# Kernel optimization log

Measured on AMD Instinct MI355X. Metric: run time of the kernel, lower is better.

The kernel has to match this reference:

```python
import jax, jax.numpy as jnp
import numpy as np

N_NODES = 50000
N_EDGES = 800000
NFEAT, NHID, NOUT = 128, 128, 64


def _glorot(key, shape):
    lim = 1.0 / np.sqrt(shape[0])
    return jax.random.uniform(key, shape, jnp.float32, -lim, lim)


def setup_inputs() -> dict:
    key = jax.random.key(0)
    ks = jax.random.split(key, 12)
    x = jax.random.normal(ks[0], (N_NODES, NFEAT), jnp.float32)
    edge_src = jax.random.randint(ks[1], (N_EDGES,), 0, N_NODES, jnp.int32)
    edge_dst = jax.random.randint(ks[2], (N_EDGES,), 0, N_NODES, jnp.int32)
    edge_w = jax.random.uniform(ks[3], (N_EDGES,), jnp.float32)  # normalized adj values
    # layer params: nfeat->nhid, nhid->nhid, nhid->nhid, nhid->nout
    W0, b0 = _glorot(ks[4], (NFEAT, NHID)), jnp.zeros((NHID,), jnp.float32)
    W1, b1 = _glorot(ks[5], (NHID, NHID)), jnp.zeros((NHID,), jnp.float32)
    W2, b2 = _glorot(ks[6], (NHID, NHID)), jnp.zeros((NHID,), jnp.float32)
    W3, b3 = _glorot(ks[7], (NHID, NOUT)), jnp.zeros((NOUT,), jnp.float32)
    return dict(x=x, edge_src=edge_src, edge_dst=edge_dst, edge_w=edge_w,
                W0=W0, b0=b0, W1=W1, b1=b1, W2=W2, b2=b2, W3=W3, b3=b3)


def _gcn_layer(h, src, dst, w, W, b):
    # support = h @ W ; out = A @ support + b  (A given as weighted edge list)
    support = h @ W                               # [N, d_out]
    msgs = support[src] * w[:, None]              # [E, d_out] gather + scale
    agg = jax.ops.segment_sum(msgs, dst, num_segments=N_NODES)  # scatter-add
    return agg + b


def reference(x, edge_src, edge_dst, edge_w, W0, b0, W1, b1, W2, b2, W3, b3):
    # eval mode: dropout is identity
    h = jax.nn.relu(_gcn_layer(x, edge_src, edge_dst, edge_w, W0, b0))
    h = jax.nn.relu(_gcn_layer(h, edge_src, edge_dst, edge_w, W1, b1))
    h = jax.nn.relu(_gcn_layer(h, edge_src, edge_dst, edge_w, W2, b2))
    h = _gcn_layer(h, edge_src, edge_dst, edge_w, W3, b3)  # no relu on last layer
    return h
```

## Files before the change

### kernel.cpp

```cpp
#include <hip/hip_runtime.h>


constexpr int NN = 50000;
constexpr int NE = 800000;
constexpr int NB = (NN + 127) >> 7;
constexpr int CAP = 4608;
constexpr int PART_CHUNK = 4096;
constexpr int PART_GRID = (NE + PART_CHUNK - 1) / PART_CHUNK;

typedef __attribute__((ext_vector_type(8))) short bf16x8;
typedef __attribute__((ext_vector_type(4))) float floatx4;
typedef __attribute__((ext_vector_type(2))) float floatx2;

__device__ inline unsigned short f2bf(float f) {
    unsigned u = __float_as_uint(f);
    u += 0x7fffu + ((u >> 16) & 1u);
    return (unsigned short)(u >> 16);
}
__device__ inline float bflo(unsigned v) { return __uint_as_float(v << 16); }
__device__ inline float bfhi(unsigned v) { return __uint_as_float(v & 0xffff0000u); }
__device__ inline unsigned char f2fp8(float f) {
    return (unsigned char)(__builtin_amdgcn_cvt_pk_fp8_f32(f, f, 0, false) & 0xff);
}


__global__ __launch_bounds__(256) void k_part(
        const int* __restrict__ src, const int* __restrict__ dst,
        const float* __restrict__ w, int* __restrict__ bfill,
        int2* __restrict__ ep) {
    __shared__ int hist[NB], base[NB], off[NB];
    int tid = threadIdx.x;
    for (int b = tid; b < NB; b += 256) { hist[b] = 0; off[b] = 0; }
    __syncthreads();

    int e0 = blockIdx.x * PART_CHUNK;
    int  sreg[16]; int wreg[16]; short breg[16];
#pragma unroll
    for (int i = 0; i < 16; ++i) {
        int e = e0 + i * 256 + tid;
        if (e < NE) {
            int d = dst[e];
            int b = d >> 7;
            sreg[i] = (src[e] & 0xffff) | ((d & 127) << 16);
            wreg[i] = __float_as_int(w[e]);
            breg[i] = (short)b;
            atomicAdd(&hist[b], 1);
        } else breg[i] = -1;
    }
    __syncthreads();
    for (int b = tid; b < NB; b += 256)
        base[b] = b * CAP + atomicAdd(&bfill[b], hist[b]);
    __syncthreads();
#pragma unroll
    for (int i = 0; i < 16; ++i) {
        if (breg[i] >= 0) {
            int b = breg[i];
            int p = atomicAdd(&off[b], 1);
            ep[base[b] + p] = make_int2(sreg[i], wreg[i]);
        }
    }
}

__global__ __launch_bounds__(256) void k_sort(
        const int2* __restrict__ ep, const int* __restrict__ bfill,
        unsigned* __restrict__ es, int2* __restrict__ begend) {
    __shared__ int cnt[128], base[128], fl[128];
    __shared__ int s_total;
    int b  = blockIdx.x;
    int n0 = b << 7;
    int nn = min(128, NN - n0);
    int t  = threadIdx.x;
    if (t < 128) { cnt[t] = 0; fl[t] = 0; }
    __syncthreads();
    int bbase = b * CAP;
    int beg = bbase, end = bbase + bfill[b];
    for (int e = beg + t; e < end; e += 256)
        atomicAdd(&cnt[(ep[e].x >> 16) & 127], 1);
    __syncthreads();
    int cp = (t < 128) ? ((cnt[t] + 15) & ~15) : 0;
    if (t < 128) base[t] = cp;
    __syncthreads();
    for (int off = 1; off < 128; off <<= 1) {
        int add = (t >= off && t < 128) ? base[t - off] : 0;
        __syncthreads();
        if (t < 128) base[t] += add;
        __syncthreads();
    }
    if (t == 127) s_total = base[127];
    __syncthreads();
    int total = s_total;
    for (int i = t; i < total + 16; i += 256) es[bbase + i] = 0u;
    if (t < nn) {
        int off = base[t] - cp;
        begend[n0 + t] = make_int2(bbase + off, bbase + off + cp);
    }
    __syncthreads();
    for (int e = beg + t; e < end; e += 256) {
        int2 v = ep[e];
        int d = (v.x >> 16) & 127;
        int off = base[d] - ((cnt[d] + 15) & ~15);
        int pos = bbase + off + atomicAdd(&fl[d], 1);
        es[pos] = (unsigned)(v.x & 0xffff) |
                  ((unsigned)f2bf(__int_as_float(v.y)) << 16);
    }
}


__global__ void k_prep(
        const float* __restrict__ W0, const float* __restrict__ W1,
        const float* __restrict__ W2, const float* __restrict__ W3,
        unsigned short* __restrict__ T0, unsigned short* __restrict__ T1,
        unsigned short* __restrict__ T2, unsigned short* __restrict__ T3,
        int* __restrict__ bfill) {
    int b = blockIdx.x;
    if (b == 448) {
        for (int i = threadIdx.x; i < NB; i += 128) bfill[i] = 0;
        return;
    }
    const float* W; unsigned short* T; int N, n;
    if (b < 128)      { W = W0; T = T0; N = 128; n = b; }
    else if (b < 256) { W = W1; T = T1; N = 128; n = b - 128; }
    else if (b < 384) { W = W2; T = T2; N = 128; n = b - 256; }
    else              { W = W3; T = T3; N = 64;  n = b - 384; }
    int k = threadIdx.x;
    T[n * 128 + k] = f2bf(W[(size_t)k * N + n]);
}


__device__ inline bf16x8 ldA_f32(const float* A, size_t off) {
    float4 u = *(const float4*)&A[off];
    float4 v = *(const float4*)&A[off + 4];
    bf16x8 r;
    r[0] = (short)f2bf(u.x); r[1] = (short)f2bf(u.y);
    r[2] = (short)f2bf(u.z); r[3] = (short)f2bf(u.w);
    r[4] = (short)f2bf(v.x); r[5] = (short)f2bf(v.y);
    r[6] = (short)f2bf(v.z); r[7] = (short)f2bf(v.w);
    return r;
}

__global__ __launch_bounds__(256) void k_gemm0(
        const float* __restrict__ A,
        const unsigned short* __restrict__ Wt,
        unsigned char* __restrict__ C,
        int M) {
    constexpr int STR = 136;
    __shared__ unsigned short sWt[128 * STR];

    const int tid = threadIdx.x;
#pragma unroll
    for (int i = 0; i < 8; ++i) {
        int c = i * 256 + tid;
        int row = c >> 4, col = (c & 15) * 8;
        *(uint4*)&sWt[row * STR + col] = *(const uint4*)&Wt[row * 128 + col];
    }

    const int wv = tid >> 6;
    const int ln = tid & 63;
    const int m  = ln & 15;
    const int qd = ln >> 4;

    int gr  = blockIdx.x * 64 + wv * 16 + m;
    int grc = (gr < M) ? gr : (M - 1);
    bf16x8 af[4];
#pragma unroll
    for (int s = 0; s < 4; ++s)
        af[s] = ldA_f32(A, (size_t)grc * 128 + s * 32 + qd * 8);

    __syncthreads();

    floatx4 acc[8];
#pragma unroll
    for (int c = 0; c < 8; ++c) {
        acc[c] = (floatx4){0.f, 0.f, 0.f, 0.f};
#pragma unroll
        for (int s = 0; s < 4; ++s) {
            bf16x8 bf = *(const bf16x8*)&sWt[(c * 16 + m) * STR + s * 32 + qd * 8];
            acc[c] = __builtin_amdgcn_mfma_f32_16x16x32_bf16(af[s], bf, acc[c], 0, 0, 0);
        }
    }

    int row0 = blockIdx.x * 64 + wv * 16 + qd * 4;
#pragma unroll
    for (int c = 0; c < 8; ++c)
#pragma unroll
        for (int r = 0; r < 4; ++r) {
            int row = row0 + r;
            if (row < M) C[(size_t)row * 128 + c * 16 + m] = f2fp8(acc[c][r]);
        }
}


#define FMAP8(W, R)                                                             \
    { floatx2 p0 = __builtin_amdgcn_cvt_pk_f32_fp8((int)(R).x, false);          \
      floatx2 p1 = __builtin_amdgcn_cvt_pk_f32_fp8((int)(R).x, true);           \
      floatx2 p2 = __builtin_amdgcn_cvt_pk_f32_fp8((int)(R).y, false);          \
      floatx2 p3 = __builtin_amdgcn_cvt_pk_f32_fp8((int)(R).y, true);           \
      acc[0] = fmaf(W, p0.x, acc[0]); acc[1] = fmaf(W, p0.y, acc[1]);           \
      acc[2] = fmaf(W, p1.x, acc[2]); acc[3] = fmaf(W, p1.y, acc[3]);           \
      acc[4] = fmaf(W, p2.x, acc[4]); acc[5] = fmaf(W, p2.y, acc[5]);           \
      acc[6] = fmaf(W, p3.x, acc[6]); acc[7] = fmaf(W, p3.y, acc[7]); }

template<int NOUT, typename CT>
__global__ __launch_bounds__(128, 4) void k_fused(
        const unsigned char* __restrict__ sup,
        const int2* __restrict__ begend, const unsigned* __restrict__ es,
        const float* __restrict__ bias,
        const unsigned short* __restrict__ Wt,
        CT* __restrict__ C,
        int M) {
    constexpr int NT  = NOUT / 16;
    constexpr int STR = 136;
    __shared__ unsigned short hT[16 * STR];

    const int tid = threadIdx.x;
    const int wv  = tid >> 6;
    const int ln  = tid & 63;
    const int g   = ln >> 4;
    const int l   = ln & 15;

    const int n0 = blockIdx.x * 16;
    int2 be = begend[n0 + wv * 8];

    for (int nn = 0; nn < 8; ++nn) {
        int n = n0 + wv * 8 + nn;
        int beg = be.x, endp = be.y;
        if (nn < 7) be = begend[n + 1];
        float acc[8] = {0.f, 0.f, 0.f, 0.f, 0.f, 0.f, 0.f, 0.f};
        if (endp > beg) {
            int e = beg;
            uint4 mv = *(const uint4*)&es[e + 4 * g];
            for (;;) {
                uint2 r0 = *(const uint2*)&sup[(size_t)(mv.x & 0xffffu) * 128 + l * 8];
                uint2 r1 = *(const uint2*)&sup[(size_t)(mv.y & 0xffffu) * 128 + l * 8];
                uint2 r2 = *(const uint2*)&sup[(size_t)(mv.z & 0xffffu) * 128 + l * 8];
                uint2 r3 = *(const uint2*)&sup[(size_t)(mv.w & 0xffffu) * 128 + l * 8];
                float w0 = bfhi(mv.x), w1 = bfhi(mv.y);
                float w2 = bfhi(mv.z), w3 = bfhi(mv.w);
                e += 16;
                bool more = e < endp;
                uint4 mn = *(const uint4*)&es[e + 4 * g];
                FMAP8(w0, r0); FMAP8(w1, r1); FMAP8(w2, r2); FMAP8(w3, r3);
                mv = mn;
                if (!more) break;
            }
#pragma unroll
            for (int f = 0; f < 8; ++f) {
                acc[f] += __shfl_xor(acc[f], 16, 64);
                acc[f] += __shfl_xor(acc[f], 32, 64);
            }
        }
        if (g == 0) {
            unsigned pk[4];
#pragma unroll
            for (int q = 0; q < 4; ++q) {
                float a0 = fmaxf(acc[2 * q]     + bias[l * 8 + 2 * q],     0.f);
                float a1 = fmaxf(acc[2 * q + 1] + bias[l * 8 + 2 * q + 1], 0.f);
                pk[q] = (unsigned)f2bf(a0) | ((unsigned)f2bf(a1) << 16);
            }
            *(uint4*)&hT[(wv * 8 + nn) * STR + l * 8] = *(uint4*)pk;
        }
    }
    __syncthreads();

    const int m_ = ln & 15, qd = ln >> 4;
    const int c0 = wv * (NT / 2);
    bf16x8 af[4];
#pragma unroll
    for (int s = 0; s < 4; ++s)
        af[s] = *(const bf16x8*)&hT[m_ * STR + s * 32 + qd * 8];

    floatx4 acc2[NT / 2];
#pragma unroll
    for (int c = 0; c < NT / 2; ++c) {
        acc2[c] = (floatx4){0.f, 0.f, 0.f, 0.f};
#pragma unroll
        for (int s = 0; s < 4; ++s) {
            bf16x8 bf = *(const bf16x8*)&Wt[(size_t)((c0 + c) * 16 + m_) * 128 + s * 32 + qd * 8];
            acc2[c] = __builtin_amdgcn_mfma_f32_16x16x32_bf16(af[s], bf, acc2[c], 0, 0, 0);
        }
    }
    int row0 = n0 + qd * 4;
#pragma unroll
    for (int c = 0; c < NT / 2; ++c)
#pragma unroll
        for (int r = 0; r < 4; ++r) {
            int row = row0 + r;
            if (row < M) {
                if constexpr (sizeof(CT) == 1)
                    C[(size_t)row * NOUT + (c0 + c) * 16 + m_] = (CT)f2fp8(acc2[c][r]);
                else
                    C[(size_t)row * NOUT + (c0 + c) * 16 + m_] = (CT)f2bf(acc2[c][r]);
            }
        }
}


#define FMA8(W, R)                                                              \
    acc[0] = fmaf(W, bflo((R).x), acc[0]); acc[1] = fmaf(W, bfhi((R).x), acc[1]); \
    acc[2] = fmaf(W, bflo((R).y), acc[2]); acc[3] = fmaf(W, bfhi((R).y), acc[3]); \
    acc[4] = fmaf(W, bflo((R).z), acc[4]); acc[5] = fmaf(W, bfhi((R).z), acc[5]); \
    acc[6] = fmaf(W, bflo((R).w), acc[6]); acc[7] = fmaf(W, bfhi((R).w), acc[7]);

__global__ __launch_bounds__(256, 4) void k_agg64(
        const unsigned short* __restrict__ sup,
        const int2* __restrict__ begend, const unsigned* __restrict__ es,
        const float* __restrict__ bias, float* __restrict__ out) {
    int n  = blockIdx.x * 4 + (threadIdx.x >> 6);
    int ln = threadIdx.x & 63;
    int g  = ln >> 3, l = ln & 7;
    int2 be = begend[n];
    int beg = be.x, endp = be.y;
    float acc[8] = {0.f, 0.f, 0.f, 0.f, 0.f, 0.f, 0.f, 0.f};
    if (endp > beg) {
        int e = beg;
        uint2 mv = *(const uint2*)&es[e + 2 * g];
        for (;;) {
            uint4 r0 = *(const uint4*)&sup[(size_t)(mv.x & 0xffffu) * 64 + l * 8];
            uint4 r1 = *(const uint4*)&sup[(size_t)(mv.y & 0xffffu) * 64 + l * 8];
            float w0 = bfhi(mv.x), w1 = bfhi(mv.y);
            e += 16;
            bool more = e < endp;
            uint2 mn = *(const uint2*)&es[e + 2 * g];
            FMA8(w0, r0); FMA8(w1, r1);
            mv = mn;
            if (!more) break;
        }
    }
#pragma unroll
    for (int f = 0; f < 8; ++f) {
        acc[f] += __shfl_xor(acc[f], 8, 64);
        acc[f] += __shfl_xor(acc[f], 16, 64);
        acc[f] += __shfl_xor(acc[f], 32, 64);
    }
    if (g == 0) {
        float4 o0 = make_float4(acc[0] + bias[l * 8],     acc[1] + bias[l * 8 + 1],
                                acc[2] + bias[l * 8 + 2], acc[3] + bias[l * 8 + 3]);
        float4 o1 = make_float4(acc[4] + bias[l * 8 + 4], acc[5] + bias[l * 8 + 5],
                                acc[6] + bias[l * 8 + 6], acc[7] + bias[l * 8 + 7]);
        *(float4*)&out[(size_t)n * 64 + l * 8]     = o0;
        *(float4*)&out[(size_t)n * 64 + l * 8 + 4] = o1;
    }
}


extern "C" void kernel_launch(void* const* d_in, const int* in_sizes, int n_in,
                              void* d_out, int out_size, void* d_ws, size_t ws_size,
                              hipStream_t stream) {
    (void)in_sizes; (void)n_in; (void)out_size; (void)ws_size;

    const float* x    = (const float*)d_in[0];
    const int*   esrc = (const int*)d_in[1];
    const int*   edst = (const int*)d_in[2];
    const float* ew   = (const float*)d_in[3];
    const float* W0   = (const float*)d_in[4];
    const float* b0   = (const float*)d_in[5];
    const float* W1   = (const float*)d_in[6];
    const float* b1   = (const float*)d_in[7];
    const float* W2   = (const float*)d_in[8];
    const float* b2   = (const float*)d_in[9];
    const float* W3   = (const float*)d_in[10];
    const float* b3   = (const float*)d_in[11];

    char* p = (char*)d_ws;
    auto alloc = [&](size_t bytes) {
        char* r = p;
        p += (bytes + 511) & ~size_t(511);
        return r;
    };
    int*      bfill  = (int*)     alloc((size_t)NB * 4);
    int2*     begend = (int2*)    alloc((size_t)NN * 8);
    int2*     ep     = (int2*)    alloc((size_t)NB * CAP * 8);
    unsigned* es     = (unsigned*)alloc((size_t)NB * CAP * 4);
    unsigned char*  s8a = (unsigned char*) alloc((size_t)NN * 128);
    unsigned char*  s8b = (unsigned char*) alloc((size_t)NN * 128);
    unsigned short* s16 = (unsigned short*)alloc((size_t)NN * 64 * 2);
    unsigned short* Wt0 = (unsigned short*)alloc((size_t)128 * 128 * 2);
    unsigned short* Wt1 = (unsigned short*)alloc((size_t)128 * 128 * 2);
    unsigned short* Wt2 = (unsigned short*)alloc((size_t)128 * 128 * 2);
    unsigned short* Wt3 = (unsigned short*)alloc((size_t)64 * 128 * 2);

    k_prep<<<449, 128, 0, stream>>>(W0, W1, W2, W3, Wt0, Wt1, Wt2, Wt3, bfill);
    k_part<<<PART_GRID, 256, 0, stream>>>(esrc, edst, ew, bfill, ep);
    k_sort<<<NB, 256, 0, stream>>>(ep, bfill, es, begend);

    const int g0_grid = (NN + 63) / 64;
    const int f_grid  = (NN + 15) / 16;
    const int a_grid  = (NN + 3) / 4;

    k_gemm0<<<g0_grid, 256, 0, stream>>>(x, Wt0, s8a, NN);
    k_fused<128, unsigned char><<<f_grid, 128, 0, stream>>>(s8a, begend, es, b0, Wt1, s8b, NN);
    k_fused<128, unsigned char><<<f_grid, 128, 0, stream>>>(s8b, begend, es, b1, Wt2, s8a, NN);
    k_fused<64, unsigned short><<<f_grid, 128, 0, stream>>>(s8a, begend, es, b2, Wt3, s16, NN);
    k_agg64<<<a_grid, 256, 0, stream>>>(s16, begend, es, b3, (float*)d_out);
}
```

Baseline: 239.4 us.

## Unfuse aggregation and GEMM, split support features into column slices

Replaces the fused aggregate-then-GEMM kernel with separate aggregation and MFMA GEMM kernels, and stores the support matrices as two column slices. Each aggregation block handles one slice, so every gathered row is narrower and the working set of the random gather is halved per pass, which should help cache hit rates. Nontemporal loads and stores are used for edge metadata and the intermediate hidden buffer. The cost is an extra bf16 hidden buffer written and re-read between kernels, plus more kernel launches.

```diff
diff --git a/kernel.cpp b/kernel.cpp
--- a/kernel.cpp
+++ b/kernel.cpp
@@ -11,6 +11,7 @@
 typedef __attribute__((ext_vector_type(8))) short bf16x8;
 typedef __attribute__((ext_vector_type(4))) float floatx4;
 typedef __attribute__((ext_vector_type(2))) float floatx2;
+typedef __attribute__((ext_vector_type(4))) unsigned int uintx4;
 
 __device__ inline unsigned short f2bf(float f) {
     unsigned u = __float_as_uint(f);
@@ -185,7 +186,77 @@
 #pragma unroll
         for (int r = 0; r < 4; ++r) {
             int row = row0 + r;
-            if (row < M) C[(size_t)row * 128 + c * 16 + m] = f2fp8(acc[c][r]);
+            if (row < M) {
+                int col = c * 16 + m;
+                int sl  = col >> 6;
+                C[(size_t)sl * NN * 64 + (size_t)row * 64 + (col & 63)] =
+                    f2fp8(acc[c][r]);
+            }
+        }
+}
+
+
+template<int NO, typename CT>
+__global__ __launch_bounds__(256) void k_gemmh(
+        const unsigned short* __restrict__ A,
+        const unsigned short* __restrict__ Wt,
+        CT* __restrict__ C,
+        int M) {
+    constexpr int STR = 136;
+    __shared__ unsigned short sWt[NO * STR];
+
+    const int tid = threadIdx.x;
+#pragma unroll
+    for (int i = 0; i < NO / 16; ++i) {
+        int c = i * 256 + tid;
+        int row = c >> 4, col = (c & 15) * 8;
+        *(uint4*)&sWt[row * STR + col] = *(const uint4*)&Wt[row * 128 + col];
+    }
+
+    const int wv = tid >> 6;
+    const int ln = tid & 63;
+    const int m  = ln & 15;
+    const int qd = ln >> 4;
+
+    int gr  = blockIdx.x * 64 + wv * 16 + m;
+    int grc = (gr < M) ? gr : (M - 1);
+    bf16x8 af[4];
+#pragma unroll
+    for (int s = 0; s < 4; ++s)
+        af[s] = __builtin_nontemporal_load(
+            (const bf16x8*)&A[(size_t)grc * 128 + s * 32 + qd * 8]);
+
+    __syncthreads();
+
+    floatx4 acc[NO / 16];
+#pragma unroll
+    for (int c = 0; c < NO / 16; ++c) {
+        acc[c] = (floatx4){0.f, 0.f, 0.f, 0.f};
+#pragma unroll
+        for (int s = 0; s < 4; ++s) {
+            bf16x8 bf = *(const bf16x8*)&sWt[(c * 16 + m) * STR + s * 32 + qd * 8];
+            acc[c] = __builtin_amdgcn_mfma_f32_16x16x32_bf16(af[s], bf, acc[c], 0, 0, 0);
+        }
+    }
+
+    int row0 = blockIdx.x * 64 + wv * 16 + qd * 4;
+#pragma unroll
+    for (int c = 0; c < NO / 16; ++c)
+#pragma unroll
+        for (int r = 0; r < 4; ++r) {
+            int row = row0 + r;
+            if (row < M) {
+                int col = c * 16 + m;
+                if constexpr (sizeof(CT) == 1) {
+                    int sl = col >> 6;
+                    C[(size_t)sl * NN * 64 + (size_t)row * 64 + (col & 63)] =
+                        (CT)f2fp8(acc[c][r]);
+                } else {
+                    int sl = col >> 5;
+                    C[(size_t)sl * NN * 32 + (size_t)row * 32 + (col & 31)] =
+                        (CT)f2bf(acc[c][r]);
+                }
+            }
         }
 }
 
@@ -200,145 +271,131 @@
       acc[4] = fmaf(W, p2.x, acc[4]); acc[5] = fmaf(W, p2.y, acc[5]);           \
       acc[6] = fmaf(W, p3.x, acc[6]); acc[7] = fmaf(W, p3.y, acc[7]); }
 
-template<int NOUT, typename CT>
-__global__ __launch_bounds__(128, 4) void k_fused(
+__global__ __launch_bounds__(128, 8) void k_aggh(
         const unsigned char* __restrict__ sup,
         const int2* __restrict__ begend, const unsigned* __restrict__ es,
         const float* __restrict__ bias,
-        const unsigned short* __restrict__ Wt,
-        CT* __restrict__ C,
-        int M) {
-    constexpr int NT  = NOUT / 16;
-    constexpr int STR = 136;
-    __shared__ unsigned short hT[16 * STR];
-
-    const int tid = threadIdx.x;
-    const int wv  = tid >> 6;
-    const int ln  = tid & 63;
-    const int g   = ln >> 4;
-    const int l   = ln & 15;
-
-    const int n0 = blockIdx.x * 16;
-    int2 be = begend[n0 + wv * 8];
+        unsigned short* __restrict__ h) {
+    const int bid  = blockIdx.x;
+    const int sl   = bid & 1;
+    const int tile = bid >> 1;
+    const int tid  = threadIdx.x;
+    const int wv = tid >> 6, ln = tid & 63;
+    const int g = ln >> 3, l = ln & 7;
+    const unsigned char* supS = sup + (size_t)sl * NN * 64;
+    const float* biasS = bias + sl * 64;
+
+    const int n0 = tile * 16 + wv * 8;
+    unsigned long long beq = __builtin_nontemporal_load(
+        (const unsigned long long*)&begend[n0]);
 
     for (int nn = 0; nn < 8; ++nn) {
-        int n = n0 + wv * 8 + nn;
-        int beg = be.x, endp = be.y;
-        if (nn < 7) be = begend[n + 1];
+        const int n = n0 + nn;
+        int beg  = (int)(unsigned)beq;
+        int endp = (int)(unsigned)(beq >> 32);
+        if (nn < 7)
+            beq = __builtin_nontemporal_load(
+                (const unsigned long long*)&begend[n + 1]);
         float acc[8] = {0.f, 0.f, 0.f, 0.f, 0.f, 0.f, 0.f, 0.f};
         if (endp > beg) {
             int e = beg;
-            uint4 mv = *(const uint4*)&es[e + 4 * g];
+            unsigned long long mv = __builtin_nontemporal_load(
+                (const unsigned long long*)&es[e + 2 * g]);
             for (;;) {
-                uint2 r0 = *(const uint2*)&sup[(size_t)(mv.x & 0xffffu) * 128 + l * 8];
-                uint2 r1 = *(const uint2*)&sup[(size_t)(mv.y & 0xffffu) * 128 + l * 8];
-                uint2 r2 = *(const uint2*)&sup[(size_t)(mv.z & 0xffffu) * 128 + l * 8];
-                uint2 r3 = *(const uint2*)&sup[(size_t)(mv.w & 0xffffu) * 128 + l * 8];
-                float w0 = bfhi(mv.x), w1 = bfhi(mv.y);
-                float w2 = bfhi(mv.z), w3 = bfhi(mv.w);
+                unsigned lo = (unsigned)mv, hi = (unsigned)(mv >> 32);
+                uint2 r0 = *(const uint2*)&supS[(size_t)(lo & 0xffffu) * 64 + l * 8];
+                uint2 r1 = *(const uint2*)&supS[(size_t)(hi & 0xffffu) * 64 + l * 8];
+                float w0 = bfhi(lo), w1 = bfhi(hi);
                 e += 16;
                 bool more = e < endp;
-                uint4 mn = *(const uint4*)&es[e + 4 * g];
-                FMAP8(w0, r0); FMAP8(w1, r1); FMAP8(w2, r2); FMAP8(w3, r3);
+                unsigned long long mn = __builtin_nontemporal_load(
+                    (const unsigned long long*)&es[e + 2 * g]);
+                FMAP8(w0, r0); FMAP8(w1, r1);
                 mv = mn;
                 if (!more) break;
             }
 #pragma unroll
             for (int f = 0; f < 8; ++f) {
+                acc[f] += __shfl_xor(acc[f], 8, 64);
                 acc[f] += __shfl_xor(acc[f], 16, 64);
                 acc[f] += __shfl_xor(acc[f], 32, 64);
             }
         }
         if (g == 0) {
-            unsigned pk[4];
+            uintx4 pk;
 #pragma unroll
             for (int q = 0; q < 4; ++q) {
-                float a0 = fmaxf(acc[2 * q]     + bias[l * 8 + 2 * q],     0.f);
-                float a1 = fmaxf(acc[2 * q + 1] + bias[l * 8 + 2 * q + 1], 0.f);
+                float a0 = fmaxf(acc[2 * q]     + biasS[l * 8 + 2 * q],     0.f);
+                float a1 = fmaxf(acc[2 * q + 1] + biasS[l * 8 + 2 * q + 1], 0.f);
                 pk[q] = (unsigned)f2bf(a0) | ((unsigned)f2bf(a1) << 16);
             }
-            *(uint4*)&hT[(wv * 8 + nn) * STR + l * 8] = *(uint4*)pk;
-        }
-    }
-    __syncthreads();
-
-    const int m_ = ln & 15, qd = ln >> 4;
-    const int c0 = wv * (NT / 2);
-    bf16x8 af[4];
-#pragma unroll
-    for (int s = 0; s < 4; ++s)
-        af[s] = *(const bf16x8*)&hT[m_ * STR + s * 32 + qd * 8];
-
-    floatx4 acc2[NT / 2];
-#pragma unroll
-    for (int c = 0; c < NT / 2; ++c) {
-        acc2[c] = (floatx4){0.f, 0.f, 0.f, 0.f};
-#pragma unroll
-        for (int s = 0; s < 4; ++s) {
-            bf16x8 bf = *(const bf16x8*)&Wt[(size_t)((c0 + c) * 16 + m_) * 128 + s * 32 + qd * 8];
-            acc2[c] = __builtin_amdgcn_mfma_f32_16x16x32_bf16(af[s], bf, acc2[c], 0, 0, 0);
-        }
-    }
-    int row0 = n0 + qd * 4;
-#pragma unroll
-    for (int c = 0; c < NT / 2; ++c)
-#pragma unroll
-        for (int r = 0; r < 4; ++r) {
-            int row = row0 + r;
-            if (row < M) {
-                if constexpr (sizeof(CT) == 1)
-                    C[(size_t)row * NOUT + (c0 + c) * 16 + m_] = (CT)f2fp8(acc2[c][r]);
-                else
-                    C[(size_t)row * NOUT + (c0 + c) * 16 + m_] = (CT)f2bf(acc2[c][r]);
-            }
-        }
-}
-
-
-#define FMA8(W, R)                                                              \
+            __builtin_nontemporal_store(
+                pk, (uintx4*)&h[(size_t)n * 128 + sl * 64 + l * 8]);
+        }
+    }
+}
+
+
+#define FMA4(W, R)                                                              \
     acc[0] = fmaf(W, bflo((R).x), acc[0]); acc[1] = fmaf(W, bfhi((R).x), acc[1]); \
-    acc[2] = fmaf(W, bflo((R).y), acc[2]); acc[3] = fmaf(W, bfhi((R).y), acc[3]); \
-    acc[4] = fmaf(W, bflo((R).z), acc[4]); acc[5] = fmaf(W, bfhi((R).z), acc[5]); \
-    acc[6] = fmaf(W, bflo((R).w), acc[6]); acc[7] = fmaf(W, bfhi((R).w), acc[7]);
-
-__global__ __launch_bounds__(256, 4) void k_agg64(
+    acc[2] = fmaf(W, bflo((R).y), acc[2]); acc[3] = fmaf(W, bfhi((R).y), acc[3]);
+
+__global__ __launch_bounds__(128, 8) void k_aggo(
         const unsigned short* __restrict__ sup,
         const int2* __restrict__ begend, const unsigned* __restrict__ es,
         const float* __restrict__ bias, float* __restrict__ out) {
-    int n  = blockIdx.x * 4 + (threadIdx.x >> 6);
-    int ln = threadIdx.x & 63;
-    int g  = ln >> 3, l = ln & 7;
-    int2 be = begend[n];
-    int beg = be.x, endp = be.y;
-    float acc[8] = {0.f, 0.f, 0.f, 0.f, 0.f, 0.f, 0.f, 0.f};
-    if (endp > beg) {
-        int e = beg;
-        uint2 mv = *(const uint2*)&es[e + 2 * g];
-        for (;;) {
-            uint4 r0 = *(const uint4*)&sup[(size_t)(mv.x & 0xffffu) * 64 + l * 8];
-            uint4 r1 = *(const uint4*)&sup[(size_t)(mv.y & 0xffffu) * 64 + l * 8];
-            float w0 = bfhi(mv.x), w1 = bfhi(mv.y);
-            e += 16;
-            bool more = e < endp;
-            uint2 mn = *(const uint2*)&es[e + 2 * g];
-            FMA8(w0, r0); FMA8(w1, r1);
-            mv = mn;
-            if (!more) break;
-        }
-    }
-#pragma unroll
-    for (int f = 0; f < 8; ++f) {
-        acc[f] += __shfl_xor(acc[f], 8, 64);
-        acc[f] += __shfl_xor(acc[f], 16, 64);
-        acc[f] += __shfl_xor(acc[f], 32, 64);
-    }
-    if (g == 0) {
-        float4 o0 = make_float4(acc[0] + bias[l * 8],     acc[1] + bias[l * 8 + 1],
-                                acc[2] + bias[l * 8 + 2], acc[3] + bias[l * 8 + 3]);
-        float4 o1 = make_float4(acc[4] + bias[l * 8 + 4], acc[5] + bias[l * 8 + 5],
-                                acc[6] + bias[l * 8 + 6], acc[7] + bias[l * 8 + 7]);
-        *(float4*)&out[(size_t)n * 64 + l * 8]     = o0;
-        *(float4*)&out[(size_t)n * 64 + l * 8 + 4] = o1;
+    const int bid  = blockIdx.x;
+    const int sl   = bid & 1;
+    const int tile = bid >> 1;
+    const int tid  = threadIdx.x;
+    const int wv = tid >> 6, ln = tid & 63;
+    const int g = ln >> 3, l = ln & 7;
+    const unsigned short* supS = sup + (size_t)sl * NN * 32;
+    const float* biasS = bias + sl * 32;
+
+    const int n0 = tile * 16 + wv * 8;
+    unsigned long long beq = __builtin_nontemporal_load(
+        (const unsigned long long*)&begend[n0]);
+
+    for (int nn = 0; nn < 8; ++nn) {
+        const int n = n0 + nn;
+        int beg  = (int)(unsigned)beq;
+        int endp = (int)(unsigned)(beq >> 32);
+        if (nn < 7)
+            beq = __builtin_nontemporal_load(
+                (const unsigned long long*)&begend[n + 1]);
+        float acc[4] = {0.f, 0.f, 0.f, 0.f};
+        if (endp > beg) {
+            int e = beg;
+            unsigned long long mv = __builtin_nontemporal_load(
+                (const unsigned long long*)&es[e + 2 * g]);
+            for (;;) {
+                unsigned lo = (unsigned)mv, hi = (unsigned)(mv >> 32);
+                uint2 r0 = *(const uint2*)&supS[(size_t)(lo & 0xffffu) * 32 + l * 4];
+                uint2 r1 = *(const uint2*)&supS[(size_t)(hi & 0xffffu) * 32 + l * 4];
+                float w0 = bfhi(lo), w1 = bfhi(hi);
+                e += 16;
+                bool more = e < endp;
+                unsigned long long mn = __builtin_nontemporal_load(
+                    (const unsigned long long*)&es[e + 2 * g]);
+                FMA4(w0, r0); FMA4(w1, r1);
+                mv = mn;
+                if (!more) break;
+            }
+#pragma unroll
+            for (int f = 0; f < 4; ++f) {
+                acc[f] += __shfl_xor(acc[f], 8, 64);
+                acc[f] += __shfl_xor(acc[f], 16, 64);
+                acc[f] += __shfl_xor(acc[f], 32, 64);
+            }
+        }
+        if (g == 0) {
+            float4 o = make_float4(acc[0] + biasS[l * 4],
+                                   acc[1] + biasS[l * 4 + 1],
+                                   acc[2] + biasS[l * 4 + 2],
+                                   acc[3] + biasS[l * 4 + 3]);
+            *(float4*)&out[(size_t)n * 64 + sl * 32 + l * 4] = o;
+        }
     }
 }
 
@@ -371,9 +428,10 @@
     int2*     begend = (int2*)    alloc((size_t)NN * 8);
     int2*     ep     = (int2*)    alloc((size_t)NB * CAP * 8);
     unsigned* es     = (unsigned*)alloc((size_t)NB * CAP * 4);
-    unsigned char*  s8a = (unsigned char*) alloc((size_t)NN * 128);
-    unsigned char*  s8b = (unsigned char*) alloc((size_t)NN * 128);
-    unsigned short* s16 = (unsigned short*)alloc((size_t)NN * 64 * 2);
+    unsigned char*  s8a  = (unsigned char*) alloc((size_t)NN * 128);
+    unsigned char*  s8b  = (unsigned char*) alloc((size_t)NN * 128);
+    unsigned short* s16  = (unsigned short*)alloc((size_t)NN * 64 * 2);
+    unsigned short* hbuf = (unsigned short*)alloc((size_t)NN * 128 * 2);
     unsigned short* Wt0 = (unsigned short*)alloc((size_t)128 * 128 * 2);
     unsigned short* Wt1 = (unsigned short*)alloc((size_t)128 * 128 * 2);
     unsigned short* Wt2 = (unsigned short*)alloc((size_t)128 * 128 * 2);
@@ -383,13 +441,15 @@
     k_part<<<PART_GRID, 256, 0, stream>>>(esrc, edst, ew, bfill, ep);
     k_sort<<<NB, 256, 0, stream>>>(ep, bfill, es, begend);
 
-    const int g0_grid = (NN + 63) / 64;
-    const int f_grid  = (NN + 15) / 16;
-    const int a_grid  = (NN + 3) / 4;
-
-    k_gemm0<<<g0_grid, 256, 0, stream>>>(x, Wt0, s8a, NN);
-    k_fused<128, unsigned char><<<f_grid, 128, 0, stream>>>(s8a, begend, es, b0, Wt1, s8b, NN);
-    k_fused<128, unsigned char><<<f_grid, 128, 0, stream>>>(s8b, begend, es, b1, Wt2, s8a, NN);
-    k_fused<64, unsigned short><<<f_grid, 128, 0, stream>>>(s8a, begend, es, b2, Wt3, s16, NN);
-    k_agg64<<<a_grid, 256, 0, stream>>>(s16, begend, es, b3, (float*)d_out);
-}
+    const int g_gemm = (NN + 63) / 64;
+    const int g_agg  = (NN / 16) * 2;
+
+    k_gemm0<<<g_gemm, 256, 0, stream>>>(x, Wt0, s8a, NN);
+    k_aggh<<<g_agg, 128, 0, stream>>>(s8a, begend, es, b0, hbuf);
+    k_gemmh<128, unsigned char><<<g_gemm, 256, 0, stream>>>(hbuf, Wt1, s8b, NN);
+    k_aggh<<<g_agg, 128, 0, stream>>>(s8b, begend, es, b1, hbuf);
+    k_gemmh<128, unsigned char><<<g_gemm, 256, 0, stream>>>(hbuf, Wt2, s8a, NN);
+    k_aggh<<<g_agg, 128, 0, stream>>>(s8a, begend, es, b2, hbuf);
+    k_gemmh<64, unsigned short><<<g_gemm, 256, 0, stream>>>(hbuf, Wt3, s16, NN);
+    k_aggo<<<g_agg, 128, 0, stream>>>(s16, begend, es, b3, (float*)d_out);
+}
```

Result: slower. 331.7 us (+38.5%).

## Assign one node per 16-lane group in aggregation kernels, 256-thread blocks

Applied to the files above, without the earlier changes.

The fused aggregate+GEMM kernels and the final 64-wide aggregation now map each node to 16 lanes. Each lane walks that node's edges eight at a time with non-temporal index loads, instead of a wave looping serially over eight nodes and reducing across lane groups with shuffles. The fused kernel's blocks grow to 256 threads so 16 nodes aggregate concurrently, and the MFMA output tiles are split across four waves. Inactive lanes read a zeroed dummy edge region appended to the edge array. This removes the per-node serial loop and the cross-lane reductions. The cost is more loop iterations, since a wave runs until the highest-degree of its four nodes is done, plus more registers for eight in-flight gathers.

```diff
diff --git a/kernel.cpp b/kernel.cpp
--- a/kernel.cpp
+++ b/kernel.cpp
@@ -7,10 +7,12 @@
 constexpr int CAP = 4608;
 constexpr int PART_CHUNK = 4096;
 constexpr int PART_GRID = (NE + PART_CHUNK - 1) / PART_CHUNK;
+constexpr int ZOFF = NB * CAP;
 
 typedef __attribute__((ext_vector_type(8))) short bf16x8;
 typedef __attribute__((ext_vector_type(4))) float floatx4;
 typedef __attribute__((ext_vector_type(2))) float floatx2;
+typedef __attribute__((ext_vector_type(4))) unsigned int uintx4;
 
 __device__ inline unsigned short f2bf(float f) {
     unsigned u = __float_as_uint(f);
@@ -111,10 +113,11 @@
         const float* __restrict__ W2, const float* __restrict__ W3,
         unsigned short* __restrict__ T0, unsigned short* __restrict__ T1,
         unsigned short* __restrict__ T2, unsigned short* __restrict__ T3,
-        int* __restrict__ bfill) {
+        int* __restrict__ bfill, unsigned* __restrict__ es) {
     int b = blockIdx.x;
     if (b == 448) {
         for (int i = threadIdx.x; i < NB; i += 128) bfill[i] = 0;
+        if (threadIdx.x < 16) es[ZOFF + threadIdx.x] = 0u;
         return;
     }
     const float* W; unsigned short* T; int N, n;
@@ -200,8 +203,11 @@
       acc[4] = fmaf(W, p2.x, acc[4]); acc[5] = fmaf(W, p2.y, acc[5]);           \
       acc[6] = fmaf(W, p3.x, acc[6]); acc[7] = fmaf(W, p3.y, acc[7]); }
 
+#define GATHF(R, MV)                                                            \
+    uint2 R = *(const uint2*)&sup[(size_t)((MV) & 0xffffu) * 128 + l * 8];
+
 template<int NOUT, typename CT>
-__global__ __launch_bounds__(128, 4) void k_fused(
+__global__ __launch_bounds__(256) void k_fused(
         const unsigned char* __restrict__ sup,
         const int2* __restrict__ begend, const unsigned* __restrict__ es,
         const float* __restrict__ bias,
@@ -213,65 +219,61 @@
     __shared__ unsigned short hT[16 * STR];
 
     const int tid = threadIdx.x;
-    const int wv  = tid >> 6;
-    const int ln  = tid & 63;
-    const int g   = ln >> 4;
-    const int l   = ln & 15;
-
-    const int n0 = blockIdx.x * 16;
-    int2 be = begend[n0 + wv * 8];
-
-    for (int nn = 0; nn < 8; ++nn) {
-        int n = n0 + wv * 8 + nn;
-        int beg = be.x, endp = be.y;
-        if (nn < 7) be = begend[n + 1];
-        float acc[8] = {0.f, 0.f, 0.f, 0.f, 0.f, 0.f, 0.f, 0.f};
-        if (endp > beg) {
-            int e = beg;
-            uint4 mv = *(const uint4*)&es[e + 4 * g];
-            for (;;) {
-                uint2 r0 = *(const uint2*)&sup[(size_t)(mv.x & 0xffffu) * 128 + l * 8];
-                uint2 r1 = *(const uint2*)&sup[(size_t)(mv.y & 0xffffu) * 128 + l * 8];
-                uint2 r2 = *(const uint2*)&sup[(size_t)(mv.z & 0xffffu) * 128 + l * 8];
-                uint2 r3 = *(const uint2*)&sup[(size_t)(mv.w & 0xffffu) * 128 + l * 8];
-                float w0 = bfhi(mv.x), w1 = bfhi(mv.y);
-                float w2 = bfhi(mv.z), w3 = bfhi(mv.w);
-                e += 16;
-                bool more = e < endp;
-                uint4 mn = *(const uint4*)&es[e + 4 * g];
-                FMAP8(w0, r0); FMAP8(w1, r1); FMAP8(w2, r2); FMAP8(w3, r3);
-                mv = mn;
-                if (!more) break;
-            }
-#pragma unroll
-            for (int f = 0; f < 8; ++f) {
-                acc[f] += __shfl_xor(acc[f], 16, 64);
-                acc[f] += __shfl_xor(acc[f], 32, 64);
-            }
-        }
-        if (g == 0) {
-            unsigned pk[4];
-#pragma unroll
-            for (int q = 0; q < 4; ++q) {
-                float a0 = fmaxf(acc[2 * q]     + bias[l * 8 + 2 * q],     0.f);
-                float a1 = fmaxf(acc[2 * q + 1] + bias[l * 8 + 2 * q + 1], 0.f);
-                pk[q] = (unsigned)f2bf(a0) | ((unsigned)f2bf(a1) << 16);
-            }
-            *(uint4*)&hT[(wv * 8 + nn) * STR + l * 8] = *(uint4*)pk;
-        }
-    }
-    __syncthreads();
-
+    const int l   = tid & 15;
+    const int n0  = blockIdx.x * 16;
+    const int n   = n0 + (tid >> 4);
+    const bool nv = n < NN;
+
+    int2 be = nv ? begend[n] : make_int2(0, 0);
+    const int en = be.y;
+    int e = be.x;
+    float acc[8] = {0.f, 0.f, 0.f, 0.f, 0.f, 0.f, 0.f, 0.f};
+    bool v = e < en;
+    if (__any(v)) {
+        int ei = v ? e : ZOFF;
+        uintx4 m0 = __builtin_nontemporal_load((const uintx4*)&es[ei]);
+        uintx4 m1 = __builtin_nontemporal_load((const uintx4*)&es[ei + 4]);
+        for (;;) {
+            GATHF(r0, m0[0]); GATHF(r1, m0[1]); GATHF(r2, m0[2]); GATHF(r3, m0[3]);
+            GATHF(r4, m1[0]); GATHF(r5, m1[1]); GATHF(r6, m1[2]); GATHF(r7, m1[3]);
+            float w0 = bfhi(m0[0]), w1 = bfhi(m0[1]), w2 = bfhi(m0[2]), w3 = bfhi(m0[3]);
+            float w4 = bfhi(m1[0]), w5 = bfhi(m1[1]), w6 = bfhi(m1[2]), w7 = bfhi(m1[3]);
+            e += 8;
+            v = e < en;
+            bool more = __any(v);
+            int eo = v ? e : ZOFF;
+            uintx4 p0 = __builtin_nontemporal_load((const uintx4*)&es[eo]);
+            uintx4 p1 = __builtin_nontemporal_load((const uintx4*)&es[eo + 4]);
+            FMAP8(w0, r0); FMAP8(w1, r1); FMAP8(w2, r2); FMAP8(w3, r3);
+            FMAP8(w4, r4); FMAP8(w5, r5); FMAP8(w6, r6); FMAP8(w7, r7);
+            m0 = p0; m1 = p1;
+            if (!more) break;
+        }
+    }
+    {
+        uintx4 pk;
+#pragma unroll
+        for (int q = 0; q < 4; ++q) {
+            float a0 = fmaxf(acc[2 * q]     + bias[l * 8 + 2 * q],     0.f);
+            float a1 = fmaxf(acc[2 * q + 1] + bias[l * 8 + 2 * q + 1], 0.f);
+            pk[q] = (unsigned)f2bf(a0) | ((unsigned)f2bf(a1) << 16);
+        }
+        *(uintx4*)&hT[(tid >> 4) * STR + l * 8] = pk;
+    }
+    __syncthreads();
+
+    const int wv = tid >> 6;
+    const int ln = tid & 63;
     const int m_ = ln & 15, qd = ln >> 4;
-    const int c0 = wv * (NT / 2);
+    const int c0 = wv * (NT / 4);
     bf16x8 af[4];
 #pragma unroll
     for (int s = 0; s < 4; ++s)
         af[s] = *(const bf16x8*)&hT[m_ * STR + s * 32 + qd * 8];
 
-    floatx4 acc2[NT / 2];
-#pragma unroll
-    for (int c = 0; c < NT / 2; ++c) {
+    floatx4 acc2[NT / 4];
+#pragma unroll
+    for (int c = 0; c < NT / 4; ++c) {
         acc2[c] = (floatx4){0.f, 0.f, 0.f, 0.f};
 #pragma unroll
         for (int s = 0; s < 4; ++s) {
@@ -281,7 +283,7 @@
     }
     int row0 = n0 + qd * 4;
 #pragma unroll
-    for (int c = 0; c < NT / 2; ++c)
+    for (int c = 0; c < NT / 4; ++c)
 #pragma unroll
         for (int r = 0; r < 4; ++r) {
             int row = row0 + r;
@@ -295,50 +297,52 @@
 }
 
 
-#define FMA8(W, R)                                                              \
+#define FMA4(W, R)                                                              \
     acc[0] = fmaf(W, bflo((R).x), acc[0]); acc[1] = fmaf(W, bfhi((R).x), acc[1]); \
-    acc[2] = fmaf(W, bflo((R).y), acc[2]); acc[3] = fmaf(W, bfhi((R).y), acc[3]); \
-    acc[4] = fmaf(W, bflo((R).z), acc[4]); acc[5] = fmaf(W, bfhi((R).z), acc[5]); \
-    acc[6] = fmaf(W, bflo((R).w), acc[6]); acc[7] = fmaf(W, bfhi((R).w), acc[7]);
-
-__global__ __launch_bounds__(256, 4) void k_agg64(
+    acc[2] = fmaf(W, bflo((R).y), acc[2]); acc[3] = fmaf(W, bfhi((R).y), acc[3]);
+
+#define GATHO(R, MV)                                                            \
+    uint2 R = *(const uint2*)&sup[(size_t)((MV) & 0xffffu) * 64 + l * 4];
+
+__global__ __launch_bounds__(256) void k_agg64(
         const unsigned short* __restrict__ sup,
         const int2* __restrict__ begend, const unsigned* __restrict__ es,
         const float* __restrict__ bias, float* __restrict__ out) {
-    int n  = blockIdx.x * 4 + (threadIdx.x >> 6);
-    int ln = threadIdx.x & 63;
-    int g  = ln >> 3, l = ln & 7;
-    int2 be = begend[n];
-    int beg = be.x, endp = be.y;
-    float acc[8] = {0.f, 0.f, 0.f, 0.f, 0.f, 0.f, 0.f, 0.f};
-    if (endp > beg) {
-        int e = beg;
-        uint2 mv = *(const uint2*)&es[e + 2 * g];
+    const int tid = threadIdx.x;
+    const int l   = tid & 15;
+    const int n   = blockIdx.x * 16 + (tid >> 4);
+    const bool nv = n < NN;
+
+    int2 be = nv ? begend[n] : make_int2(0, 0);
+    const int en = be.y;
+    int e = be.x;
+    float acc[4] = {0.f, 0.f, 0.f, 0.f};
+    bool v = e < en;
+    if (__any(v)) {
+        int ei = v ? e : ZOFF;
+        uintx4 m0 = __builtin_nontemporal_load((const uintx4*)&es[ei]);
+        uintx4 m1 = __builtin_nontemporal_load((const uintx4*)&es[ei + 4]);
         for (;;) {
-            uint4 r0 = *(const uint4*)&sup[(size_t)(mv.x & 0xffffu) * 64 + l * 8];
-            uint4 r1 = *(const uint4*)&sup[(size_t)(mv.y & 0xffffu) * 64 + l * 8];
-            float w0 = bfhi(mv.x), w1 = bfhi(mv.y);
-            e += 16;
-            bool more = e < endp;
-            uint2 mn = *(const uint2*)&es[e + 2 * g];
-            FMA8(w0, r0); FMA8(w1, r1);
-            mv = mn;
+            GATHO(r0, m0[0]); GATHO(r1, m0[1]); GATHO(r2, m0[2]); GATHO(r3, m0[3]);
+            GATHO(r4, m1[0]); GATHO(r5, m1[1]); GATHO(r6, m1[2]); GATHO(r7, m1[3]);
+            float w0 = bfhi(m0[0]), w1 = bfhi(m0[1]), w2 = bfhi(m0[2]), w3 = bfhi(m0[3]);
+            float w4 = bfhi(m1[0]), w5 = bfhi(m1[1]), w6 = bfhi(m1[2]), w7 = bfhi(m1[3]);
+            e += 8;
+            v = e < en;
+            bool more = __any(v);
+            int eo = v ? e : ZOFF;
+            uintx4 p0 = __builtin_nontemporal_load((const uintx4*)&es[eo]);
+            uintx4 p1 = __builtin_nontemporal_load((const uintx4*)&es[eo + 4]);
+            FMA4(w0, r0); FMA4(w1, r1); FMA4(w2, r2); FMA4(w3, r3);
+            FMA4(w4, r4); FMA4(w5, r5); FMA4(w6, r6); FMA4(w7, r7);
+            m0 = p0; m1 = p1;
             if (!more) break;
         }
     }
-#pragma unroll
-    for (int f = 0; f < 8; ++f) {
-        acc[f] += __shfl_xor(acc[f], 8, 64);
-        acc[f] += __shfl_xor(acc[f], 16, 64);
-        acc[f] += __shfl_xor(acc[f], 32, 64);
-    }
-    if (g == 0) {
-        float4 o0 = make_float4(acc[0] + bias[l * 8],     acc[1] + bias[l * 8 + 1],
-                                acc[2] + bias[l * 8 + 2], acc[3] + bias[l * 8 + 3]);
-        float4 o1 = make_float4(acc[4] + bias[l * 8 + 4], acc[5] + bias[l * 8 + 5],
-                                acc[6] + bias[l * 8 + 6], acc[7] + bias[l * 8 + 7]);
-        *(float4*)&out[(size_t)n * 64 + l * 8]     = o0;
-        *(float4*)&out[(size_t)n * 64 + l * 8 + 4] = o1;
+    if (nv) {
+        float4 o = make_float4(acc[0] + bias[l * 4],     acc[1] + bias[l * 4 + 1],
+                               acc[2] + bias[l * 4 + 2], acc[3] + bias[l * 4 + 3]);
+        *(float4*)&out[(size_t)n * 64 + l * 4] = o;
     }
 }
 
@@ -370,7 +374,7 @@
     int*      bfill  = (int*)     alloc((size_t)NB * 4);
     int2*     begend = (int2*)    alloc((size_t)NN * 8);
     int2*     ep     = (int2*)    alloc((size_t)NB * CAP * 8);
-    unsigned* es     = (unsigned*)alloc((size_t)NB * CAP * 4);
+    unsigned* es     = (unsigned*)alloc(((size_t)NB * CAP + 64) * 4);
     unsigned char*  s8a = (unsigned char*) alloc((size_t)NN * 128);
     unsigned char*  s8b = (unsigned char*) alloc((size_t)NN * 128);
     unsigned short* s16 = (unsigned short*)alloc((size_t)NN * 64 * 2);
@@ -379,17 +383,17 @@
     unsigned short* Wt2 = (unsigned short*)alloc((size_t)128 * 128 * 2);
     unsigned short* Wt3 = (unsigned short*)alloc((size_t)64 * 128 * 2);
 
-    k_prep<<<449, 128, 0, stream>>>(W0, W1, W2, W3, Wt0, Wt1, Wt2, Wt3, bfill);
+    k_prep<<<449, 128, 0, stream>>>(W0, W1, W2, W3, Wt0, Wt1, Wt2, Wt3,
+                                    bfill, es);
     k_part<<<PART_GRID, 256, 0, stream>>>(esrc, edst, ew, bfill, ep);
     k_sort<<<NB, 256, 0, stream>>>(ep, bfill, es, begend);
 
-    const int g0_grid = (NN + 63) / 64;
-    const int f_grid  = (NN + 15) / 16;
-    const int a_grid  = (NN + 3) / 4;
-
-    k_gemm0<<<g0_grid, 256, 0, stream>>>(x, Wt0, s8a, NN);
-    k_fused<128, unsigned char><<<f_grid, 128, 0, stream>>>(s8a, begend, es, b0, Wt1, s8b, NN);
-    k_fused<128, unsigned char><<<f_grid, 128, 0, stream>>>(s8b, begend, es, b1, Wt2, s8a, NN);
-    k_fused<64, unsigned short><<<f_grid, 128, 0, stream>>>(s8a, begend, es, b2, Wt3, s16, NN);
-    k_agg64<<<a_grid, 256, 0, stream>>>(s16, begend, es, b3, (float*)d_out);
-}
+    const int g_gemm = (NN + 63) / 64;
+    const int f_grid = (NN + 15) / 16;
+
+    k_gemm0<<<g_gemm, 256, 0, stream>>>(x, Wt0, s8a, NN);
+    k_fused<128, unsigned char><<<f_grid, 256, 0, stream>>>(s8a, begend, es, b0, Wt1, s8b, NN);
+    k_fused<128, unsigned char><<<f_grid, 256, 0, stream>>>(s8b, begend, es, b1, Wt2, s8a, NN);
+    k_fused<64, unsigned short><<<f_grid, 256, 0, stream>>>(s8a, begend, es, b2, Wt3, s16, NN);
+    k_agg64<<<f_grid, 256, 0, stream>>>(s16, begend, es, b3, (float*)d_out);
+}
```

Result: no change. 240.6 us (+0.5%).
